# Kernel optimization log

Measured on AMD Instinct MI355X. Metric: run time of the kernel, lower is better.

The kernel has to match this reference:

```python
import jax, jax.numpy as jnp
import numpy as np
from jax import lax

NUM_SUPERNODES = 1024
KNN_K = 16
MIN_GRIPPER = 16
MIN_MASK = 8
GRIP_START = 0
GRIP_RADIUS = 0.1
NEG_INF = -jnp.inf


def _take(a, idx):
    return jnp.take_along_axis(a, idx, axis=1)


def _scatter_or(idx, keep, Bf, N):
    # OR `keep` into a fresh [Bf,N] bool mask at positions idx (mirrors torch scatter_)
    b = jnp.arange(Bf)[:, None]
    return jnp.zeros((Bf, N), dtype=bool).at[b, idx].max(keep)


def _cdist(a, b):
    # a [B,M,3], b [B,N,3] -> [B,M,N] euclidean
    d2 = (jnp.sum(a * a, -1)[:, :, None] + jnp.sum(b * b, -1)[:, None, :]
          - 2.0 * jnp.einsum('bmd,bnd->bmn', a, b))
    return jnp.sqrt(jnp.maximum(d2, 0.0))


def _sample_supernodes(xyz, valid, state, mask_id, extra_scores, global_scores):
    Bf, N, _ = xyz.shape
    M = NUM_SUPERNODES
    valid = valid.astype(bool)
    row_has_valid = valid.any(axis=1)
    first_valid = jnp.argmax(valid, axis=1).astype(jnp.int32)  # [Bf]

    # ---- gripper quota: nearest points to gripper xyz (within radius if any) ----
    k_grip = min(MIN_GRIPPER, M)
    gxyz = state[:, GRIP_START:GRIP_START + 3]
    gdist = jnp.linalg.norm(xyz - gxyz[:, None, :], axis=-1)  # [Bf,N]
    in_radius = gdist <= GRIP_RADIUS
    has_radius = (valid & in_radius).any(axis=1, keepdims=True)
    eligible = valid & (in_radius | ~has_radius)
    dist_rank = jnp.where(eligible, gdist, jnp.inf)
    neg_vals, grip_idx = lax.top_k(-dist_rank, k_grip)
    grip_vals = -neg_vals
    grip_keep = jnp.isfinite(grip_vals) & row_has_valid[:, None]
    head_idx = jnp.where(grip_keep, grip_idx, first_valid[:, None])
    head_bucket = jnp.where(grip_keep, 1, -1)
    selected = _scatter_or(grip_idx, grip_keep, Bf, N)

    remaining = M - k_grip
    # ---- mask-instance quota: one point per mask id (dedup via sort) ----
    mask_cand = valid & ~selected
    sentinel = jnp.iinfo(mask_id.dtype).max
    mask_key = jnp.where(mask_cand, mask_id, sentinel)
    sort_idx = jnp.argsort(mask_key, axis=1)
    sorted_valid = _take(mask_cand, sort_idx)
    sorted_mask = _take(mask_id, sort_idx)
    first_for_id = jnp.concatenate(
        [sorted_valid[:, :1],
         sorted_valid[:, 1:] & (sorted_mask[:, 1:] != sorted_mask[:, :-1])], axis=1)
    pos = jnp.arange(N, dtype=jnp.float32)[None, :]
    mask_scores = jnp.where(first_for_id, -pos, NEG_INF)
    mask_vals, mask_pos = lax.top_k(mask_scores, remaining)
    mask_idx = _take(sort_idx, mask_pos)
    mask_keep = jnp.isfinite(mask_vals) & row_has_valid[:, None]
    selected_after_mask = selected | _scatter_or(mask_idx, mask_keep, Bf, N)

    # ---- extra random mask supernodes to guarantee min_mask quota ----
    k_extra = min(MIN_MASK, remaining)
    es = jnp.where(valid & ~selected_after_mask, extra_scores, NEG_INF)
    extra_vals, extra_idx = lax.top_k(es, k_extra)
    extra_keep = jnp.isfinite(extra_vals) & row_has_valid[:, None]
    use_extra = ~mask_keep[:, :k_extra] & extra_keep
    mask_idx = mask_idx.at[:, :k_extra].set(
        jnp.where(use_extra, extra_idx, mask_idx[:, :k_extra]))
    mask_keep = mask_keep.at[:, :k_extra].set(mask_keep[:, :k_extra] | use_extra)

    # ---- global random fill ----
    selected_for_global = selected | _scatter_or(mask_idx, mask_keep, Bf, N)
    gs = jnp.where(valid & ~selected_for_global, global_scores, NEG_INF)
    gvals, gidx = lax.top_k(gs, remaining)
    gkeep = jnp.isfinite(gvals) & row_has_valid[:, None]
    fill_idx = jnp.where(mask_keep, mask_idx,
                         jnp.where(gkeep, gidx, first_valid[:, None]))
    fill_bucket = jnp.where(mask_keep, 2, jnp.where(gkeep, 0, -1))

    out_idx = jnp.concatenate([head_idx, fill_idx], axis=1)
    out_bucket = jnp.concatenate([head_bucket, fill_bucket], axis=1)
    out_valid = _take(valid, out_idx) & row_has_valid[:, None]
    out_bucket = jnp.where(out_valid, out_bucket, -1)
    return out_idx, out_valid, out_bucket


def setup_inputs() -> dict:
    key = jax.random.key(0)
    ks = jax.random.split(key, 6)
    Bf, N, C = 8, 16384, 64
    return {
        'x': jax.random.normal(ks[0], (Bf, N, C), dtype=jnp.float32),
        'xyz': jax.random.normal(ks[1], (Bf, N, 3), dtype=jnp.float32),
        'valid': jnp.ones((Bf, N), dtype=bool),
        'state': jax.random.normal(ks[2], (Bf, 8), dtype=jnp.float32),
        'mask_id': jax.random.randint(ks[3], (Bf, N), 0, 32, dtype=jnp.int32),
        'extra_scores': jax.random.uniform(ks[4], (Bf, N), dtype=jnp.float32),
        'global_scores': jax.random.uniform(ks[5], (Bf, N), dtype=jnp.float32),
    }


def reference(x, xyz, valid, state, mask_id, extra_scores, global_scores):
    Bf, N, C = x.shape
    out_idx, out_valid, out_bucket = _sample_supernodes(
        xyz, valid, state, mask_id, extra_scores, global_scores)
    # gather_points
    supernode_xyz = _take(xyz, out_idx[:, :, None].repeat(3, axis=2))  # [Bf,M,3]
    # build_knn_neighbors: masked cdist + topk smallest
    dist = _cdist(supernode_xyz.astype(jnp.float32), xyz.astype(jnp.float32))
    dist = jnp.where(valid.astype(bool)[:, None, :], dist, jnp.inf)
    neg_vals, neighbor_idx = lax.top_k(-dist, KNN_K)
    neighbor_mask = jnp.isfinite(-neg_vals)  # [Bf,M,K]
    # gather_neighbors
    b = jnp.arange(Bf)[:, None, None]
    neighbor_feats = x[b, neighbor_idx]  # [Bf,M,K,C]
    return (neighbor_feats, supernode_xyz, neighbor_mask,
            out_idx, out_valid, out_bucket)
```

## Files before the change

kernel.cpp:

```cpp
#include <hip/hip_runtime.h>
#include <math.h>

typedef unsigned long long u64;
typedef unsigned int u32;

#define BF 8
#define NPTS 16384
#define HALFPTS 8192
#define M_SN 1024
#define CCH 64
#define KNN 16
#define NTHR1 1024
#define KPER 16
#define TBL 4096
#define CCAP 2048
#define REM 1008

constexpr size_t O0 = 0;
constexpr size_t O1 = 8388608;
constexpr size_t O2 = 8413184;
constexpr size_t O3 = 8544256;
constexpr size_t O4 = 8552448;
constexpr size_t O5 = 8560640;

#define PW_OFF ((size_t)256)
#define PW_BYTES ((size_t)BF * NPTS * 16)
#define WN_BYTES ((size_t)2 * BF * M_SN * KNN * 8)

__device__ __forceinline__ bool is_valid_el(const void* vp, int mode, long long i) {
  if (mode == 1) return ((const unsigned char*)vp)[i] != 0;
  if (mode == 2) return ((const float*)vp)[i] != 0.0f;
  return ((const int*)vp)[i] != 0;
}

__device__ __forceinline__ u32 desc_enc(float f) {
  u32 u = __float_as_uint(f);
  u32 s = (u & 0x80000000u) ? ~u : (u | 0x80000000u);
  return ~s;
}
__device__ __forceinline__ bool enc_finite(u32 d) {
  u32 s = ~d;
  u32 u = (s & 0x80000000u) ? (s & 0x7FFFFFFFu) : ~s;
  return (u & 0x7F800000u) != 0x7F800000u;
}

__device__ __forceinline__ u64 wave_min_u64(u64 v) {
#pragma unroll
  for (int d = 32; d >= 1; d >>= 1) {
    u32 lo = __shfl_xor((u32)(v & 0xFFFFFFFFu), d, 64);
    u32 hi = __shfl_xor((u32)(v >> 32), d, 64);
    u64 o = ((u64)hi << 32) | lo;
    if (o < v) v = o;
  }
  return v;
}

__device__ __forceinline__ u64 block_min_u64(u64 v, u64* red16, int t) {
  v = wave_min_u64(v);
  if ((t & 63) == 0) red16[t >> 6] = v;
  __syncthreads();
  if (t < 64) {
    u64 x = red16[t & 15];
    x = wave_min_u64(x);
    if (t == 0) red16[0] = x;
  }
  __syncthreads();
  u64 r = red16[0];
  __syncthreads();
  return r;
}

__device__ __forceinline__ int block_excl_scan(int val, int* scanb, int t, int* tot) {
  int incl = val;
#pragma unroll
  for (int d = 1; d < 64; d <<= 1) {
    int v = __shfl_up(incl, d, 64);
    if ((t & 63) >= d) incl += v;
  }
  if ((t & 63) == 63) scanb[t >> 6] = incl;
  __syncthreads();
  if (t < 64) {
    int ws = (t < 16) ? scanb[t] : 0;
#pragma unroll
    for (int d = 1; d < 16; d <<= 1) {
      int v = __shfl_up(ws, d, 64);
      if ((t & 63) >= d) ws += v;
    }
    if (t < 16) scanb[16 + t] = ws;
  }
  __syncthreads();
  int wv = t >> 6;
  int base = (wv == 0) ? 0 : scanb[16 + wv - 1];
  *tot = scanb[16 + 15];
  int r = base + incl - val;
  __syncthreads();
  return r;
}

__device__ __forceinline__ u64 shfl64_grp(u64 v, int src) {
  u32 lo = (u32)__shfl((int)(u32)(v & 0xFFFFFFFFu), src, 32);
  u32 hi = (u32)__shfl((int)(u32)(v >> 32), src, 32);
  return ((u64)hi << 32) | lo;
}

template<bool ASC, bool SHIFTBIN>
__device__ __forceinline__ void topk_select(const u32* ek, const u32* bk, u32 cmask,
    int Twant, int* table, u64* cand, int* scanb, int* sh, int* outArr, int t) {
  for (int j = t; j < TBL; j += NTHR1) table[j] = 0;
  if (t == 6) sh[6] = 0x7FFFFFFF;
  if (t == 7) sh[7] = 1;
  __syncthreads();
#pragma unroll
  for (int k = 0; k < KPER; k++) {
    if ((cmask >> k) & 1u) {
      int bin = SHIFTBIN ? (int)(ek[k] >> 20) : (int)bk[k];
      atomicAdd(&table[bin], 1);
    }
  }
  __syncthreads();
  int c_[4]; int c4 = 0;
#pragma unroll
  for (int q = 0; q < 4; q++) { c_[q] = table[4 * t + q]; c4 += c_[q]; }
  int htot;
  int cum = block_excl_scan(c4, scanb, t, &htot);
  const int T = min(Twant, htot);
  int e_ = cum;
#pragma unroll
  for (int q = 0; q < 4; q++) {
    int nx = e_ + c_[q];
    if (T > 0 && e_ < T && nx >= T) atomicMin(&sh[6], 4 * t + q);
    table[4 * t + q] = e_;
    e_ = nx;
  }
  __syncthreads();
  if (T <= 0) return;
  const int B = sh[6];
#pragma unroll
  for (int k = 0; k < KPER; k++) {
    if ((cmask >> k) & 1u) {
      int bin = SHIFTBIN ? (int)(ek[k] >> 20) : (int)bk[k];
      if (bin <= B) {
        int pos = atomicAdd(&table[bin], 1);
        if (pos < CCAP)
          cand[pos] = ((u64)ek[k] << 32) | ((u64)(u32)bin << 14) | (u32)(k * NTHR1 + t);
      }
    }
  }
  __syncthreads();
  const int nc = table[B];
  if (nc <= CCAP) {
    for (int c = t; c < nc; c += NTHR1) {
      u64 key = cand[c];
      int bin = (int)((key >> 14) & 0xFFFu);
      int s = bin ? table[bin - 1] : 0;
      int e2 = table[bin];
      int r = s;
      for (int j = s; j < e2; j++) r += (cand[j] < key);
      if (r < T) {
        u32 enc = (u32)(key >> 32);
        int ix = (int)(key & 0x3FFFu);
        bool fin = ASC ? (enc < 0x7F800000u) : enc_finite(enc);
        outArr[r] = fin ? ix : (ix | (int)0x80000000);
      }
    }
  } else {
    if (t == 0) sh[7] = 0;
  }
  __syncthreads();
}

__global__ void detect_valid(const unsigned* __restrict__ w, int nwords, int* __restrict__ flag) {
  __shared__ int cls;
  int t = threadIdx.x;
  if (t == 0) cls = 0;
  __syncthreads();
  int local = 0;
  for (int i = t; i < nwords; i += blockDim.x) {
    unsigned v = w[i];
    if (v == 0x3F800000u) local = 2;
    else if (v != 0u && v != 1u) local = max(local, 1);
  }
  if (local) atomicMax(&cls, local);
  __syncthreads();
  if (t == 0) flag[0] = cls;
}

__global__ __launch_bounds__(1024)
void sample_kernel(const float* __restrict__ xyz, const void* __restrict__ validp,
                   const float* __restrict__ state, const int* __restrict__ mask_id,
                   const float* __restrict__ extra, const float* __restrict__ glob,
                   const int* __restrict__ flagp, float4* __restrict__ pw,
                   float* __restrict__ out) {
  __shared__ u64 red16[16];
  __shared__ int table[TBL];
  __shared__ int scanb[32];
  __shared__ int mpick[REM];
  __shared__ u64 cand[CCAP];
  __shared__ int gsorted[REM];
  __shared__ int head_i[16];
  __shared__ int head_bk[16];
  __shared__ int sh[8];

  const int b = blockIdx.x, t = threadIdx.x;
  const int vmode = flagp[0];
  const float* xyzb = xyz + (size_t)b * NPTS * 3;
  const int* midb = mask_id + (size_t)b * NPTS;
  const float* exb = extra + (size_t)b * NPTS;
  const float* glb = glob + (size_t)b * NPTS;

  if (t < 8) sh[t] = 0;
  if (t == 1) sh[1] = 0x7FFFFFFF;
  if (t < 16) gsorted[t] = -1;
  __syncthreads();

  u32 vbits = 0;
#pragma unroll
  for (int k = 0; k < KPER; k++) {
    int i = k * NTHR1 + t;
    if (is_valid_el(validp, vmode, (long long)b * NPTS + i)) vbits |= 1u << k;
  }
  if (vbits) {
    atomicOr(&sh[0], 1);
    atomicMin(&sh[1], (__ffs(vbits) - 1) * NTHR1 + t);
  }

  float gx = state[b * 8 + 0], gy = state[b * 8 + 1], gz = state[b * 8 + 2];
  float gd[KPER];
  u32 inr = 0;
#pragma unroll
  for (int k = 0; k < KPER; k++) {
    int i = k * NTHR1 + t;
    float px = xyzb[3 * i], py = xyzb[3 * i + 1], pz = xyzb[3 * i + 2];
    float dx = px - gx, dy = py - gy, dz = pz - gz;
    float d = sqrtf((dx * dx + dy * dy) + dz * dz);
    gd[k] = d;
    bool vb = (vbits >> k) & 1u;
    if (vb && d <= 0.1f) inr |= 1u << k;
    if (pw) {
      float sb = __fadd_rn(__fadd_rn(__fmul_rn(px, px), __fmul_rn(py, py)), __fmul_rn(pz, pz));
      pw[(size_t)b * NPTS + i] = make_float4(px, py, pz, vb ? sb : INFINITY);
    }
  }
  if (inr) atomicOr(&sh[2], 1);
  __syncthreads();

  const int rhv = sh[0];
  const int first_valid = rhv ? sh[1] : 0;
  const u32 elig = vbits & (sh[2] ? inr : 0xFFFFu);
  u32 sel = 0;

  {
    u32 ek[KPER];
#pragma unroll
    for (int k = 0; k < KPER; k++) ek[k] = __float_as_uint(gd[k]);
    topk_select<true, true>(ek, nullptr, elig, 16, table, cand, scanb, sh, gsorted, t);
    if (sh[7]) {
      if (t < 16) {
        int g = gsorted[t];
        head_i[t] = (g >= 0) ? g : first_valid;
        head_bk[t] = (g >= 0) ? 1 : -1;
      }
      __syncthreads();
      for (int j = 0; j < 16; j++) {
        if (head_bk[j] == 1) {
          int ix = head_i[j];
          if ((ix & (NTHR1 - 1)) == t) sel |= 1u << (ix >> 10);
        }
      }
    } else {
      for (int it = 0; it < 16; ++it) {
        u64 best = ~0ull;
#pragma unroll
        for (int k = 0; k < KPER; k++) {
          if (((elig >> k) & 1u) && !((sel >> k) & 1u)) {
            u64 key = ((u64)__float_as_uint(gd[k]) << 32) | (u32)(k * NTHR1 + t);
            if (key < best) best = key;
          }
        }
        u64 w = block_min_u64(best, red16, t);
        bool keep = (w >> 32) < 0x7F800000ull;
        int idx = (int)(w & 0xFFFFFFFFu);
        if (t == 0) { head_i[it] = keep ? idx : first_valid; head_bk[it] = keep ? 1 : -1; }
        if (keep && (idx & (NTHR1 - 1)) == t) sel |= 1u << (idx >> 10);
      }
      __syncthreads();
    }
  }

  for (int j = t; j < TBL; j += NTHR1) table[j] = 0x7FFFFFFF;
  __syncthreads();
#pragma unroll
  for (int k = 0; k < KPER; k++) {
    if (((vbits >> k) & 1u) && !((sel >> k) & 1u)) {
      int i = k * NTHR1 + t;
      int id = midb[i];
      if ((u32)id < TBL) atomicMin(&table[id], i);
    }
  }
  __syncthreads();
  int cnt = 0;
#pragma unroll
  for (int q = 0; q < 4; q++) cnt += (table[4 * t + q] != 0x7FFFFFFF);
  int mtot;
  int excl = block_excl_scan(cnt, scanb, t, &mtot);
  {
    int pos = excl;
#pragma unroll
    for (int q = 0; q < 4; q++) {
      int v = table[4 * t + q];
      if (v != 0x7FFFFFFF) { if (pos < REM) mpick[pos] = v; pos++; }
    }
  }
  __syncthreads();
  const int nm = min(mtot, REM);
  for (int j = 0; j < nm; j++) {
    int p = mpick[j];
    if ((p & (NTHR1 - 1)) == t) sel |= 1u << (p >> 10);
  }

  u32 extra_used = 0;
  if (nm < 8 && rhv) {
    u32 extrbits = 0;
    for (int j = 0; j < 8; j++) {
      u64 best = ~0ull;
#pragma unroll
      for (int k = 0; k < KPER; k++) {
        if (((vbits >> k) & 1u) && !((sel >> k) & 1u) && !((extrbits >> k) & 1u)) {
          int i = k * NTHR1 + t;
          u64 key = ((u64)desc_enc(exb[i]) << 32) | (u32)i;
          if (key < best) best = key;
        }
      }
      u64 w = block_min_u64(best, red16, t);
      if (w == ~0ull) break;
      int idx = (int)(w & 0xFFFFFFFFu);
      bool fin = enc_finite((u32)(w >> 32));
      if ((idx & (NTHR1 - 1)) == t) extrbits |= 1u << (idx >> 10);
      if (j >= nm && fin) {
        extra_used |= 1u << j;
        if (t == 0) mpick[j] = idx;
        if ((idx & (NTHR1 - 1)) == t) sel |= 1u << (idx >> 10);
      }
    }
    __syncthreads();
  }

  {
    u32 cbits = vbits & ~sel;
    u32 ek[KPER], bk[KPER];
#pragma unroll
    for (int k = 0; k < KPER; k++) {
      if ((cbits >> k) & 1u) {
        float f = glb[k * NTHR1 + t];
        ek[k] = desc_enc(f);
        float g = fminf(fmaxf(f, 0.0f), 0.99999994f);
        bk[k] = 4095u - (u32)(g * 4096.0f);
      } else { ek[k] = 0xFFFFFFFFu; bk[k] = 4095u; }
    }
    for (int j = t; j < REM; j += NTHR1) gsorted[j] = -1;
    topk_select<false, false>(ek, bk, cbits, REM, table, cand, scanb, sh, gsorted, t);
    if (!sh[7]) {
      u32 gext = 0;
      for (int j = 0; j < REM; j++) {
        u64 best = ~0ull;
#pragma unroll
        for (int k = 0; k < KPER; k++) {
          if (((cbits >> k) & 1u) && !((gext >> k) & 1u)) {
            u64 key = ((u64)ek[k] << 32) | (u32)(k * NTHR1 + t);
            if (key < best) best = key;
          }
        }
        u64 w = block_min_u64(best, red16, t);
        if (w == ~0ull) break;
        int idx = (int)(w & 0xFFFFFFFFu);
        if ((idx & (NTHR1 - 1)) == t) gext |= 1u << (idx >> 10);
        if (t == 0) gsorted[j] = enc_finite((u32)(w >> 32)) ? idx : (idx | (int)0x80000000);
      }
      __syncthreads();
    }
  }

  {
    int slot = t;
    int idx, bucket;
    if (slot < 16) {
      idx = head_i[slot];
      bucket = head_bk[slot];
    } else {
      int jj = slot - 16;
      bool mk = (jj < nm) || (jj < 8 && ((extra_used >> jj) & 1u));
      if (mk) { idx = mpick[jj]; bucket = 2; }
      else {
        int g = gsorted[jj];
        if (rhv && g >= 0) { idx = g; bucket = 0; }
        else { idx = first_valid; bucket = -1; }
      }
    }
    bool ov = rhv && is_valid_el(validp, vmode, (long long)b * NPTS + idx);
    int ob = ov ? bucket : -1;
    size_t o = (size_t)b * M_SN + slot;
    out[O3 + o] = (float)idx;
    out[O4 + o] = ov ? 1.0f : 0.0f;
    out[O5 + o] = (float)ob;
    out[O1 + 3 * o + 0] = xyzb[3 * idx + 0];
    out[O1 + 3 * o + 1] = xyzb[3 * idx + 1];
    out[O1 + 3 * o + 2] = xyzb[3 * idx + 2];
  }
}

#define NTHR2 256
#define CH 1024
#define SPB 8

__global__ __launch_bounds__(256, 8)
void knn_kernel(const float* __restrict__ x, const float* __restrict__ xyz,
                const void* __restrict__ validp, const int* __restrict__ flagp,
                const float4* __restrict__ pw, u64* __restrict__ wnws,
                float* __restrict__ out) {
  __shared__ __align__(16) float4 st[CH];
  __shared__ u64 wn[SPB * KNN];

  const int b = blockIdx.x >> 7;
  const int grp = blockIdx.x & 127;
  const int half = blockIdx.y;
  const int t = threadIdx.x;
  const int sl = t >> 5;
  const int sub = t & 31;
  const int lanebase = t & 32;
  const int m = grp * SPB + sl;
  const int vmode = flagp[0];
  const float* xyzb = xyz + (size_t)b * NPTS * 3;

  const int sidx = (int)out[O3 + (size_t)b * M_SN + m];
  float ax, ay, az;
  if (pw) { float4 q = pw[(size_t)b * NPTS + sidx]; ax = q.x; ay = q.y; az = q.z; }
  else { ax = xyzb[3 * sidx]; ay = xyzb[3 * sidx + 1]; az = xyzb[3 * sidx + 2]; }
  const float sa = __fadd_rn(__fadd_rn(__fmul_rn(ax, ax), __fmul_rn(ay, ay)), __fmul_rn(az, az));

  float ld2 = INFINITY;
  int lidx = 0;
  float kth = INFINITY;

  const int cbeg = wnws ? half * HALFPTS : 0;
  const int cend = wnws ? cbeg + HALFPTS : NPTS;

  for (int c0 = cbeg; c0 < cend; c0 += CH) {
    if (pw) {
      const float4* src = pw + (size_t)b * NPTS + c0;
#pragma unroll
      for (int q = 0; q < CH / NTHR2; q++) st[t + q * NTHR2] = src[t + q * NTHR2];
    } else {
      for (int p = t; p < CH; p += NTHR2) {
        float px = xyzb[3 * (c0 + p)], py = xyzb[3 * (c0 + p) + 1], pz = xyzb[3 * (c0 + p) + 2];
        bool v = is_valid_el(validp, vmode, (long long)b * NPTS + c0 + p);
        float sb = __fadd_rn(__fadd_rn(__fmul_rn(px, px), __fmul_rn(py, py)), __fmul_rn(pz, pz));
        st[p] = make_float4(px, py, pz, v ? sb : INFINITY);
      }
    }
    __syncthreads();
#pragma unroll 4
    for (int j = 0; j < CH / 32; j++) {
      float4 v = st[sub + 32 * j];
      float dot = __fadd_rn(__fadd_rn(__fmul_rn(ax, v.x), __fmul_rn(ay, v.y)), __fmul_rn(az, v.z));
      float d2 = fmaxf(__fsub_rn(__fadd_rn(sa, v.w), __fmul_rn(2.0f, dot)), 0.0f);
      u64 bal = __ballot(d2 < kth);
      u32 mq = (u32)(bal >> lanebase);
      while (mq) {
        int bb = __ffs(mq) - 1;
        mq &= mq - 1;
        float kd = __shfl(d2, lanebase + bb, 64);
        if (kd < kth) {
          int ki = c0 + 32 * j + bb;
          bool gt = ld2 > kd;
          float sd = __shfl_up(ld2, 1, 32);
          int si = __shfl_up(lidx, 1, 32);
          int pg = __shfl_up(gt ? 1 : 0, 1, 32);
          if (sub == 0) pg = 0;
          ld2 = gt ? (pg ? sd : kd) : ld2;
          lidx = gt ? (pg ? si : ki) : lidx;
          kth = __shfl(ld2, 15, 32);
        }
      }
    }
    __syncthreads();
  }

  if (wnws) {
    if (sub < KNN)
      wnws[((size_t)half * BF + b) * M_SN * KNN + (size_t)m * KNN + sub] =
          ((u64)__float_as_uint(ld2) << 32) | (u32)lidx;
    return;
  }

  if (sub < KNN) wn[sl * KNN + sub] = ((u64)__float_as_uint(ld2) << 32) | (u32)lidx;
  __syncthreads();
  {
    int s2 = t >> 5;
    int k2 = (t >> 1) & 15;
    int hf = t & 1;
    int mm = grp * SPB + s2;
    u64 key = wn[s2 * KNN + k2];
    int ni = (int)(key & (u64)(NPTS - 1));
    size_t o2 = ((size_t)b * M_SN + mm) * KNN + k2;
    if (hf == 0) out[O2 + o2] = ((u32)(key >> 32) < 0x7F800000u) ? 1.0f : 0.0f;
    const float4* src = (const float4*)(x + ((size_t)b * NPTS + ni) * CCH);
    float4* dst = (float4*)(out + O0 + o2 * CCH);
#pragma unroll
    for (int q = 0; q < 8; q++) dst[hf * 8 + q] = src[hf * 8 + q];
  }
}

__global__ __launch_bounds__(256)
void knn_merge_kernel(const float* __restrict__ x, const u64* __restrict__ wnws,
                      float* __restrict__ out) {
  __shared__ u64 wn[SPB * KNN];
  const int b = blockIdx.x >> 7;
  const int grp = blockIdx.x & 127;
  const int t = threadIdx.x;
  const int sl = t >> 5;
  const int sub = t & 31;
  const int m = grp * SPB + sl;

  const int h = sub >> 4, k = sub & 15;
  u64 my = wnws[((size_t)h * BF + b) * M_SN * KNN + (size_t)m * KNN + k];
  const int obase = (1 - h) << 4;
  int cnt2 = 0;
#pragma unroll
  for (int j = 0; j < 16; j++) {
    u64 o = shfl64_grp(my, obase + j);
    cnt2 += h ? (o <= my) : (o < my);
  }
  int rank = k + cnt2;
  if (rank < KNN) wn[sl * KNN + rank] = my;
  __syncthreads();

  {
    int s2 = t >> 5;
    int k2 = (t >> 1) & 15;
    int hf = t & 1;
    int mm = grp * SPB + s2;
    u64 key = wn[s2 * KNN + k2];
    int ni = (int)(key & (u64)(NPTS - 1));
    size_t o2 = ((size_t)b * M_SN + mm) * KNN + k2;
    if (hf == 0) out[O2 + o2] = ((u32)(key >> 32) < 0x7F800000u) ? 1.0f : 0.0f;
    const float4* src = (const float4*)(x + ((size_t)b * NPTS + ni) * CCH);
    float4* dst = (float4*)(out + O0 + o2 * CCH);
#pragma unroll
    for (int q = 0; q < 8; q++) dst[hf * 8 + q] = src[hf * 8 + q];
  }
}

extern "C" void kernel_launch(void* const* d_in, const int* in_sizes, int n_in,
                              void* d_out, int out_size, void* d_ws, size_t ws_size,
                              hipStream_t stream) {
  const float* x = (const float*)d_in[0];
  const float* xyz = (const float*)d_in[1];
  const void* valid = d_in[2];
  const float* state = (const float*)d_in[3];
  const int* mask_id = (const int*)d_in[4];
  const float* extra = (const float*)d_in[5];
  const float* glob = (const float*)d_in[6];
  float* out = (float*)d_out;
  int* flag = (int*)d_ws;

  float4* pw = nullptr;
  u64* wnws = nullptr;
  if (ws_size >= PW_OFF + PW_BYTES) pw = (float4*)((char*)d_ws + PW_OFF);
  if (pw && ws_size >= PW_OFF + PW_BYTES + WN_BYTES)
    wnws = (u64*)((char*)d_ws + PW_OFF + PW_BYTES);

  detect_valid<<<1, 1024, 0, stream>>>((const unsigned*)valid, in_sizes[2] / 4, flag);
  sample_kernel<<<BF, NTHR1, 0, stream>>>(xyz, valid, state, mask_id, extra, glob, flag, pw, out);
  dim3 kg(BF * 128, wnws ? 2 : 1);
  knn_kernel<<<kg, NTHR2, 0, stream>>>(x, xyz, valid, flag, pw, wnws, out);
  if (wnws) knn_merge_kernel<<<BF * 128, NTHR2, 0, stream>>>(x, wnws, out);
}
```

Measured before the change: 280.6 us.

## Rewrite KNN distance as FMA score and buffer candidates per chunk

The KNN scan now ranks points by the score 2a·p − |p|² computed with fused multiply-adds, in place of the full squared distance, so the ordering becomes a max-selection. The top-16 list is seeded from a sorting network over the first 32 points. Later candidates that beat the current threshold are appended to a per-group shared-memory buffer, which is merged after each chunk, with the old per-candidate insertion kept as a fallback when the buffer overflows. This is meant to cut the serialized shuffle-insertion work inside the inner loop, at the cost of extra shared memory, lower launch-bounds occupancy, a new key encoding (desc_enc/enc_finite), and possible rounding differences in tie ordering.

```diff
diff --git a/kernel.cpp b/kernel.cpp
--- a/kernel.cpp
+++ b/kernel.cpp
@@ -411,36 +411,42 @@
 #define NTHR2 256
 #define CH 1024
 #define SPB 8
-
-__global__ __launch_bounds__(256, 8)
+#define GCAP 64
+
+__global__ __launch_bounds__(256, 4)
 void knn_kernel(const float* __restrict__ x, const float* __restrict__ xyz,
                 const void* __restrict__ validp, const int* __restrict__ flagp,
                 const float4* __restrict__ pw, u64* __restrict__ wnws,
                 float* __restrict__ out) {
   __shared__ __align__(16) float4 st[CH];
+  __shared__ float bqf[(NTHR2 / 32) * GCAP];
+  __shared__ int bqi[(NTHR2 / 32) * GCAP];
   __shared__ u64 wn[SPB * KNN];
 
   const int b = blockIdx.x >> 7;
   const int grp = blockIdx.x & 127;
   const int half = blockIdx.y;
   const int t = threadIdx.x;
-  const int sl = t >> 5;
+  const int g = t >> 5;
   const int sub = t & 31;
   const int lanebase = t & 32;
-  const int m = grp * SPB + sl;
-  const int vmode = flagp[0];
+  const int m = grp * SPB + g;
   const float* xyzb = xyz + (size_t)b * NPTS * 3;
 
   const int sidx = (int)out[O3 + (size_t)b * M_SN + m];
   float ax, ay, az;
-  if (pw) { float4 q = pw[(size_t)b * NPTS + sidx]; ax = q.x; ay = q.y; az = q.z; }
+  if (pw) { float4 qv = pw[(size_t)b * NPTS + sidx]; ax = qv.x; ay = qv.y; az = qv.z; }
   else { ax = xyzb[3 * sidx]; ay = xyzb[3 * sidx + 1]; az = xyzb[3 * sidx + 2]; }
-  const float sa = __fadd_rn(__fadd_rn(__fmul_rn(ax, ax), __fmul_rn(ay, ay)), __fmul_rn(az, az));
-
-  float ld2 = INFINITY;
-  int lidx = 0;
-  float kth = INFINITY;
-
+  const float a2x = ax + ax, a2y = ay + ay, a2z = az + az;
+
+  float ld = -INFINITY;
+  int li = 0;
+  float kq = -INFINITY;
+  int bn = 0;
+  float* gbq = bqf + g * GCAP;
+  int* gbi = bqi + g * GCAP;
+
+  const int vmode = pw ? 0 : flagp[0];
   const int cbeg = wnws ? half * HALFPTS : 0;
   const int cend = wnws ? cbeg + HALFPTS : NPTS;
 
@@ -448,7 +454,7 @@
     if (pw) {
       const float4* src = pw + (size_t)b * NPTS + c0;
 #pragma unroll
-      for (int q = 0; q < CH / NTHR2; q++) st[t + q * NTHR2] = src[t + q * NTHR2];
+      for (int qq = 0; qq < CH / NTHR2; qq++) st[t + qq * NTHR2] = src[t + qq * NTHR2];
     } else {
       for (int p = t; p < CH; p += NTHR2) {
         float px = xyzb[3 * (c0 + p)], py = xyzb[3 * (c0 + p) + 1], pz = xyzb[3 * (c0 + p) + 2];
@@ -458,41 +464,96 @@
       }
     }
     __syncthreads();
+
+    int jstart = 0;
+    if (c0 == cbeg) {
+      float4 v = st[sub];
+      float qv = __builtin_fmaf(a2x, v.x, __builtin_fmaf(a2y, v.y, __builtin_fmaf(a2z, v.z, -v.w)));
+      int qi = c0 + sub;
+#pragma unroll
+      for (int p = 0; p < 32; p++) {
+        int par;
+        if ((p & 1) == 0) par = sub ^ 1;
+        else par = (sub == 0 || sub == 31) ? sub : (((sub - 1) ^ 1) + 1);
+        float oq = __shfl(qv, par, 32);
+        int oi = __shfl(qi, par, 32);
+        if (par != sub) {
+          bool lo = sub < par;
+          bool take = lo ? (oq > qv) : (oq < qv);
+          if (take) { qv = oq; qi = oi; }
+        }
+      }
+      ld = qv; li = qi;
+      kq = __shfl(ld, 15, 32);
+      jstart = 1;
+    }
+
 #pragma unroll 4
-    for (int j = 0; j < CH / 32; j++) {
+    for (int j = jstart; j < CH / 32; j++) {
       float4 v = st[sub + 32 * j];
-      float dot = __fadd_rn(__fadd_rn(__fmul_rn(ax, v.x), __fmul_rn(ay, v.y)), __fmul_rn(az, v.z));
-      float d2 = fmaxf(__fsub_rn(__fadd_rn(sa, v.w), __fmul_rn(2.0f, dot)), 0.0f);
-      u64 bal = __ballot(d2 < kth);
-      u32 mq = (u32)(bal >> lanebase);
-      while (mq) {
-        int bb = __ffs(mq) - 1;
-        mq &= mq - 1;
-        float kd = __shfl(d2, lanebase + bb, 64);
-        if (kd < kth) {
-          int ki = c0 + 32 * j + bb;
-          bool gt = ld2 > kd;
-          float sd = __shfl_up(ld2, 1, 32);
-          int si = __shfl_up(lidx, 1, 32);
+      float qv = __builtin_fmaf(a2x, v.x, __builtin_fmaf(a2y, v.y, __builtin_fmaf(a2z, v.z, -v.w)));
+      u64 bal = __ballot(qv > kq);
+      u32 mqg = (u32)(bal >> lanebase);
+      if (mqg) {
+        if (qv > kq) {
+          int pos = bn + __popc(mqg & ((1u << sub) - 1u));
+          if (pos < GCAP) { gbq[pos] = qv; gbi[pos] = c0 + 32 * j + sub; }
+        }
+        bn += __popc(mqg);
+      }
+    }
+
+    if (bn > GCAP) {
+      for (int j = jstart; j < CH / 32; j++) {
+        float4 v = st[sub + 32 * j];
+        float qv = __builtin_fmaf(a2x, v.x, __builtin_fmaf(a2y, v.y, __builtin_fmaf(a2z, v.z, -v.w)));
+        u64 bal = __ballot(qv > kq);
+        u32 mq = (u32)(bal >> lanebase);
+        while (mq) {
+          int bb = __ffs(mq) - 1;
+          mq &= mq - 1;
+          float kd = __shfl(qv, lanebase + bb, 64);
+          if (kd > kq) {
+            int ki = c0 + 32 * j + bb;
+            bool gt = ld < kd;
+            float sd = __shfl_up(ld, 1, 32);
+            int si = __shfl_up(li, 1, 32);
+            int pg = __shfl_up(gt ? 1 : 0, 1, 32);
+            if (sub == 0) pg = 0;
+            ld = gt ? (pg ? sd : kd) : ld;
+            li = gt ? (pg ? si : ki) : li;
+            kq = __shfl(ld, 15, 32);
+          }
+        }
+      }
+    } else {
+      for (int c = 0; c < bn; c++) {
+        float kd = gbq[c];
+        int ki = gbi[c];
+        if (kd > kq) {
+          bool gt = ld < kd;
+          float sd = __shfl_up(ld, 1, 32);
+          int si = __shfl_up(li, 1, 32);
           int pg = __shfl_up(gt ? 1 : 0, 1, 32);
           if (sub == 0) pg = 0;
-          ld2 = gt ? (pg ? sd : kd) : ld2;
-          lidx = gt ? (pg ? si : ki) : lidx;
-          kth = __shfl(ld2, 15, 32);
-        }
-      }
-    }
+          ld = gt ? (pg ? sd : kd) : ld;
+          li = gt ? (pg ? si : ki) : li;
+          kq = __shfl(ld, 15, 32);
+        }
+      }
+    }
+    bn = 0;
     __syncthreads();
   }
 
   if (wnws) {
     if (sub < KNN)
       wnws[((size_t)half * BF + b) * M_SN * KNN + (size_t)m * KNN + sub] =
-          ((u64)__float_as_uint(ld2) << 32) | (u32)lidx;
+          ((u64)desc_enc(ld) << 32) | (u32)li;
     return;
   }
 
-  if (sub < KNN) wn[sl * KNN + sub] = ((u64)__float_as_uint(ld2) << 32) | (u32)lidx;
+  if (sub < KNN) wn[g * KNN + sub] = ((u64)desc_enc(ld) << 32) | (u32)li;
   __syncthreads();
   {
     int s2 = t >> 5;
@@ -502,7 +563,7 @@
     u64 key = wn[s2 * KNN + k2];
     int ni = (int)(key & (u64)(NPTS - 1));
     size_t o2 = ((size_t)b * M_SN + mm) * KNN + k2;
-    if (hf == 0) out[O2 + o2] = ((u32)(key >> 32) < 0x7F800000u) ? 1.0f : 0.0f;
+    if (hf == 0) out[O2 + o2] = enc_finite((u32)(key >> 32)) ? 1.0f : 0.0f;
     const float4* src = (const float4*)(x + ((size_t)b * NPTS + ni) * CCH);
     float4* dst = (float4*)(out + O0 + o2 * CCH);
 #pragma unroll
@@ -542,7 +603,7 @@
     u64 key = wn[s2 * KNN + k2];
     int ni = (int)(key & (u64)(NPTS - 1));
     size_t o2 = ((size_t)b * M_SN + mm) * KNN + k2;
-    if (hf == 0) out[O2 + o2] = ((u32)(key >> 32) < 0x7F800000u) ? 1.0f : 0.0f;
+    if (hf == 0) out[O2 + o2] = enc_finite((u32)(key >> 32)) ? 1.0f : 0.0f;
     const float4* src = (const float4*)(x + ((size_t)b * NPTS + ni) * CCH);
     float4* dst = (float4*)(out + O0 + o2 * CCH);
 #pragma unroll
```

New measurement: 289.6 us. 1.03x slower.

## Register-block KNN over four supernodes per warp and split points into four segments

Applied to the files above, without the earlier changes.

The KNN kernel now processes four supernodes per 32-lane group and streams points straight from global memory with a one-step register prefetch, replacing the shared-memory staging and its barriers. It scores candidates with a fused 2a·b − |b|² FMA form, seeds each list with an odd-even transposition sort, and splits the point range into four segments, with a generalized rank-based merge kernel. The valid-type detection is folded into sample_kernel, which drops one launch. Reusing each loaded point across four supernodes cuts load traffic per distance, at the cost of more registers and a heavier merge step.

```diff
diff --git a/kernel.cpp b/kernel.cpp
--- a/kernel.cpp
+++ b/kernel.cpp
@@ -6,7 +6,6 @@
 
 #define BF 8
 #define NPTS 16384
-#define HALFPTS 8192
 #define M_SN 1024
 #define CCH 64
 #define KNN 16
@@ -25,7 +24,7 @@
 
 #define PW_OFF ((size_t)256)
 #define PW_BYTES ((size_t)BF * NPTS * 16)
-#define WN_BYTES ((size_t)2 * BF * M_SN * KNN * 8)
+#define SEG1_BYTES ((size_t)BF * M_SN * KNN * 8)
 
 __device__ __forceinline__ bool is_valid_el(const void* vp, int mode, long long i) {
   if (mode == 1) return ((const unsigned char*)vp)[i] != 0;
@@ -95,12 +94,6 @@
   int r = base + incl - val;
   __syncthreads();
   return r;
-}
-
-__device__ __forceinline__ u64 shfl64_grp(u64 v, int src) {
-  u32 lo = (u32)__shfl((int)(u32)(v & 0xFFFFFFFFu), src, 32);
-  u32 hi = (u32)__shfl((int)(u32)(v >> 32), src, 32);
-  return ((u64)hi << 32) | lo;
 }
 
 template<bool ASC, bool SHIFTBIN>
@@ -189,8 +182,7 @@
 void sample_kernel(const float* __restrict__ xyz, const void* __restrict__ validp,
                    const float* __restrict__ state, const int* __restrict__ mask_id,
                    const float* __restrict__ extra, const float* __restrict__ glob,
-                   const int* __restrict__ flagp, float4* __restrict__ pw,
-                   float* __restrict__ out) {
+                   int vwords, float4* __restrict__ pw, float* __restrict__ out) {
   __shared__ u64 red16[16];
   __shared__ int table[TBL];
   __shared__ int scanb[32];
@@ -202,7 +194,6 @@
   __shared__ int sh[8];
 
   const int b = blockIdx.x, t = threadIdx.x;
-  const int vmode = flagp[0];
   const float* xyzb = xyz + (size_t)b * NPTS * 3;
   const int* midb = mask_id + (size_t)b * NPTS;
   const float* exb = extra + (size_t)b * NPTS;
@@ -212,6 +203,19 @@
   if (t == 1) sh[1] = 0x7FFFFFFF;
   if (t < 16) gsorted[t] = -1;
   __syncthreads();
+
+  {
+    const unsigned* w = (const unsigned*)validp;
+    int local = 0;
+    for (int i = t; i < vwords; i += NTHR1) {
+      unsigned vv = w[i];
+      if (vv == 0x3F800000u) local = 2;
+      else if (vv != 0u && vv != 1u) local = max(local, 1);
+    }
+    if (local) atomicMax(&sh[3], local);
+  }
+  __syncthreads();
+  const int vmode = sh[3];
 
   u32 vbits = 0;
 #pragma unroll
@@ -409,144 +413,170 @@
 }
 
 #define NTHR2 256
-#define CH 1024
-#define SPB 8
-
-__global__ __launch_bounds__(256, 8)
+#define SPG 4
+#define SNBLK 32
+
+__device__ __forceinline__ float4 load_pt(const float4* pw, const float* xyzb,
+    const void* validp, int vmode, long long gbase, int i) {
+  if (pw) return pw[gbase + i];
+  float px = xyzb[3 * i], py = xyzb[3 * i + 1], pz = xyzb[3 * i + 2];
+  bool v = is_valid_el(validp, vmode, gbase + i);
+  float sb = __fadd_rn(__fadd_rn(__fmul_rn(px, px), __fmul_rn(py, py)), __fmul_rn(pz, pz));
+  return make_float4(px, py, pz, v ? sb : INFINITY);
+}
+
+__global__ __launch_bounds__(256)
 void knn_kernel(const float* __restrict__ x, const float* __restrict__ xyz,
                 const void* __restrict__ validp, const int* __restrict__ flagp,
-                const float4* __restrict__ pw, u64* __restrict__ wnws,
+                const float4* __restrict__ pw, u64* __restrict__ wnws, int nseg,
                 float* __restrict__ out) {
-  __shared__ __align__(16) float4 st[CH];
-  __shared__ u64 wn[SPB * KNN];
-
-  const int b = blockIdx.x >> 7;
-  const int grp = blockIdx.x & 127;
-  const int half = blockIdx.y;
+  __shared__ u64 wnl[SNBLK * KNN];
+
+  const int b = blockIdx.x >> 5;
+  const int snblk = blockIdx.x & 31;
+  const int seg = blockIdx.y;
   const int t = threadIdx.x;
-  const int sl = t >> 5;
+  const int g = t >> 5;
   const int sub = t & 31;
   const int lanebase = t & 32;
-  const int m = grp * SPB + sl;
-  const int vmode = flagp[0];
+  const int m0 = snblk * SNBLK + g * SPG;
   const float* xyzb = xyz + (size_t)b * NPTS * 3;
-
-  const int sidx = (int)out[O3 + (size_t)b * M_SN + m];
-  float ax, ay, az;
-  if (pw) { float4 q = pw[(size_t)b * NPTS + sidx]; ax = q.x; ay = q.y; az = q.z; }
-  else { ax = xyzb[3 * sidx]; ay = xyzb[3 * sidx + 1]; az = xyzb[3 * sidx + 2]; }
-  const float sa = __fadd_rn(__fadd_rn(__fmul_rn(ax, ax), __fmul_rn(ay, ay)), __fmul_rn(az, az));
-
-  float ld2 = INFINITY;
-  int lidx = 0;
-  float kth = INFINITY;
-
-  const int cbeg = wnws ? half * HALFPTS : 0;
-  const int cend = wnws ? cbeg + HALFPTS : NPTS;
-
-  for (int c0 = cbeg; c0 < cend; c0 += CH) {
-    if (pw) {
-      const float4* src = pw + (size_t)b * NPTS + c0;
-#pragma unroll
-      for (int q = 0; q < CH / NTHR2; q++) st[t + q * NTHR2] = src[t + q * NTHR2];
-    } else {
-      for (int p = t; p < CH; p += NTHR2) {
-        float px = xyzb[3 * (c0 + p)], py = xyzb[3 * (c0 + p) + 1], pz = xyzb[3 * (c0 + p) + 2];
-        bool v = is_valid_el(validp, vmode, (long long)b * NPTS + c0 + p);
-        float sb = __fadd_rn(__fadd_rn(__fmul_rn(px, px), __fmul_rn(py, py)), __fmul_rn(pz, pz));
-        st[p] = make_float4(px, py, pz, v ? sb : INFINITY);
-      }
-    }
-    __syncthreads();
-#pragma unroll 4
-    for (int j = 0; j < CH / 32; j++) {
-      float4 v = st[sub + 32 * j];
-      float dot = __fadd_rn(__fadd_rn(__fmul_rn(ax, v.x), __fmul_rn(ay, v.y)), __fmul_rn(az, v.z));
-      float d2 = fmaxf(__fsub_rn(__fadd_rn(sa, v.w), __fmul_rn(2.0f, dot)), 0.0f);
-      u64 bal = __ballot(d2 < kth);
+  const long long gbase = (long long)b * NPTS;
+  const int vmode = pw ? 0 : flagp[0];
+
+  float a2x[SPG], a2y[SPG], a2z[SPG];
+#pragma unroll
+  for (int s = 0; s < SPG; s++) {
+    int sidx = (int)out[O3 + (size_t)b * M_SN + m0 + s];
+    float ax, ay, az;
+    if (pw) { float4 c = pw[gbase + sidx]; ax = c.x; ay = c.y; az = c.z; }
+    else { ax = xyzb[3 * sidx]; ay = xyzb[3 * sidx + 1]; az = xyzb[3 * sidx + 2]; }
+    a2x[s] = ax + ax; a2y[s] = ay + ay; a2z[s] = az + az;
+  }
+
+  const int S = NPTS / nseg;
+  const int sbeg = seg * S;
+  const int NJ = S / 32;
+
+  float ld[SPG]; int li[SPG]; float kq[SPG];
+
+  {
+    float4 v = load_pt(pw, xyzb, validp, vmode, gbase, sbeg + sub);
+    float qv[SPG]; int qi[SPG];
+#pragma unroll
+    for (int s = 0; s < SPG; s++) {
+      qv[s] = __builtin_fmaf(a2x[s], v.x, __builtin_fmaf(a2y[s], v.y, __builtin_fmaf(a2z[s], v.z, -v.w)));
+      qi[s] = sbeg + sub;
+    }
+#pragma unroll
+    for (int p = 0; p < 32; p++) {
+      int par;
+      if ((p & 1) == 0) par = sub ^ 1;
+      else par = (sub == 0 || sub == 31) ? sub : (((sub - 1) ^ 1) + 1);
+      bool lo = sub < par;
+#pragma unroll
+      for (int s = 0; s < SPG; s++) {
+        float oq = __shfl(qv[s], par, 32);
+        int oi = __shfl(qi[s], par, 32);
+        if (par != sub) {
+          bool take = lo ? (oq > qv[s]) : (oq < qv[s]);
+          if (take) { qv[s] = oq; qi[s] = oi; }
+        }
+      }
+    }
+#pragma unroll
+    for (int s = 0; s < SPG; s++) { ld[s] = qv[s]; li[s] = qi[s]; kq[s] = __shfl(ld[s], 15, 32); }
+  }
+
+  float4 v = load_pt(pw, xyzb, validp, vmode, gbase, sbeg + 32 * (NJ > 1 ? 1 : 0) + sub);
+  for (int j = 1; j < NJ; j++) {
+    int jn = min(j + 1, NJ - 1);
+    float4 vn = load_pt(pw, xyzb, validp, vmode, gbase, sbeg + 32 * jn + sub);
+#pragma unroll
+    for (int s = 0; s < SPG; s++) {
+      float qv = __builtin_fmaf(a2x[s], v.x, __builtin_fmaf(a2y[s], v.y, __builtin_fmaf(a2z[s], v.z, -v.w)));
+      u64 bal = __ballot(qv > kq[s]);
       u32 mq = (u32)(bal >> lanebase);
       while (mq) {
         int bb = __ffs(mq) - 1;
         mq &= mq - 1;
-        float kd = __shfl(d2, lanebase + bb, 64);
-        if (kd < kth) {
-          int ki = c0 + 32 * j + bb;
-          bool gt = ld2 > kd;
-          float sd = __shfl_up(ld2, 1, 32);
-          int si = __shfl_up(lidx, 1, 32);
+        float kd = __shfl(qv, lanebase + bb, 64);
+        if (kd > kq[s]) {
+          int ki = sbeg + 32 * j + bb;
+          bool gt = ld[s] < kd;
+          float sd = __shfl_up(ld[s], 1, 32);
+          int si = __shfl_up(li[s], 1, 32);
           int pg = __shfl_up(gt ? 1 : 0, 1, 32);
           if (sub == 0) pg = 0;
-          ld2 = gt ? (pg ? sd : kd) : ld2;
-          lidx = gt ? (pg ? si : ki) : lidx;
-          kth = __shfl(ld2, 15, 32);
+          ld[s] = gt ? (pg ? sd : kd) : ld[s];
+          li[s] = gt ? (pg ? si : ki) : li[s];
+          kq[s] = __shfl(ld[s], 15, 32);
         }
       }
     }
-    __syncthreads();
+    v = vn;
   }
 
   if (wnws) {
-    if (sub < KNN)
-      wnws[((size_t)half * BF + b) * M_SN * KNN + (size_t)m * KNN + sub] =
-          ((u64)__float_as_uint(ld2) << 32) | (u32)lidx;
+#pragma unroll
+    for (int s = 0; s < SPG; s++)
+      if (sub < KNN)
+        wnws[(((size_t)seg * BF + b) * M_SN + (m0 + s)) * KNN + sub] =
+            ((u64)desc_enc(ld[s]) << 32) | (u32)li[s];
     return;
   }
 
-  if (sub < KNN) wn[sl * KNN + sub] = ((u64)__float_as_uint(ld2) << 32) | (u32)lidx;
+#pragma unroll
+  for (int s = 0; s < SPG; s++)
+    if (sub < KNN) wnl[(g * SPG + s) * KNN + sub] = ((u64)desc_enc(ld[s]) << 32) | (u32)li[s];
+  __syncthreads();
+  for (int r = t; r < SNBLK * KNN; r += NTHR2) {
+    u64 key = wnl[r];
+    int ni = (int)(key & (u64)(NPTS - 1));
+    int mm = snblk * SNBLK + (r >> 4);
+    size_t o2 = ((size_t)b * M_SN + mm) * KNN + (r & 15);
+    out[O2 + o2] = enc_finite((u32)(key >> 32)) ? 1.0f : 0.0f;
+    const float4* src = (const float4*)(x + (gbase + ni) * CCH);
+    float4* dst = (float4*)(out + O0 + o2 * CCH);
+#pragma unroll
+    for (int q = 0; q < 16; q++) dst[q] = src[q];
+  }
+}
+
+#define MSPB 4
+__global__ __launch_bounds__(256)
+void knn_merge_kernel(const float* __restrict__ x, const u64* __restrict__ wnws,
+                      int nseg, float* __restrict__ out) {
+  __shared__ u64 keys[MSPB][64];
+  __shared__ u64 wsel[MSPB][KNN];
+  const int b = blockIdx.x >> 8;
+  const int sn0 = (blockIdx.x & 255) * MSPB;
+  const int t = threadIdx.x;
+  const int s = t >> 6, e = t & 63;
+  const int E = nseg * KNN;
+  if (e < E) {
+    int seg = e >> 4, k = e & 15;
+    keys[s][e] = wnws[(((size_t)seg * BF + b) * M_SN + sn0 + s) * KNN + k];
+  }
+  __syncthreads();
+  if (e < E) {
+    u64 my = keys[s][e];
+    int rk = 0;
+    for (int j = 0; j < E; j++) rk += (keys[s][j] < my);
+    if (rk < KNN) wsel[s][rk] = my;
+  }
   __syncthreads();
   {
-    int s2 = t >> 5;
-    int k2 = (t >> 1) & 15;
-    int hf = t & 1;
-    int mm = grp * SPB + s2;
-    u64 key = wn[s2 * KNN + k2];
+    int row = t >> 2, q4 = t & 3;
+    u64 key = wsel[row >> 4][row & 15];
     int ni = (int)(key & (u64)(NPTS - 1));
-    size_t o2 = ((size_t)b * M_SN + mm) * KNN + k2;
-    if (hf == 0) out[O2 + o2] = ((u32)(key >> 32) < 0x7F800000u) ? 1.0f : 0.0f;
+    int mm = sn0 + (row >> 4);
+    size_t o2 = ((size_t)b * M_SN + mm) * KNN + (row & 15);
+    if (q4 == 0) out[O2 + o2] = enc_finite((u32)(key >> 32)) ? 1.0f : 0.0f;
     const float4* src = (const float4*)(x + ((size_t)b * NPTS + ni) * CCH);
     float4* dst = (float4*)(out + O0 + o2 * CCH);
 #pragma unroll
-    for (int q = 0; q < 8; q++) dst[hf * 8 + q] = src[hf * 8 + q];
-  }
-}
-
-__global__ __launch_bounds__(256)
-void knn_merge_kernel(const float* __restrict__ x, const u64* __restrict__ wnws,
-                      float* __restrict__ out) {
-  __shared__ u64 wn[SPB * KNN];
-  const int b = blockIdx.x >> 7;
-  const int grp = blockIdx.x & 127;
-  const int t = threadIdx.x;
-  const int sl = t >> 5;
-  const int sub = t & 31;
-  const int m = grp * SPB + sl;
-
-  const int h = sub >> 4, k = sub & 15;
-  u64 my = wnws[((size_t)h * BF + b) * M_SN * KNN + (size_t)m * KNN + k];
-  const int obase = (1 - h) << 4;
-  int cnt2 = 0;
-#pragma unroll
-  for (int j = 0; j < 16; j++) {
-    u64 o = shfl64_grp(my, obase + j);
-    cnt2 += h ? (o <= my) : (o < my);
-  }
-  int rank = k + cnt2;
-  if (rank < KNN) wn[sl * KNN + rank] = my;
-  __syncthreads();
-
-  {
-    int s2 = t >> 5;
-    int k2 = (t >> 1) & 15;
-    int hf = t & 1;
-    int mm = grp * SPB + s2;
-    u64 key = wn[s2 * KNN + k2];
-    int ni = (int)(key & (u64)(NPTS - 1));
-    size_t o2 = ((size_t)b * M_SN + mm) * KNN + k2;
-    if (hf == 0) out[O2 + o2] = ((u32)(key >> 32) < 0x7F800000u) ? 1.0f : 0.0f;
-    const float4* src = (const float4*)(x + ((size_t)b * NPTS + ni) * CCH);
-    float4* dst = (float4*)(out + O0 + o2 * CCH);
-#pragma unroll
-    for (int q = 0; q < 8; q++) dst[hf * 8 + q] = src[hf * 8 + q];
+    for (int q = 0; q < 4; q++) dst[q4 * 4 + q] = src[q4 * 4 + q];
   }
 }
 
@@ -562,16 +592,23 @@
   const float* glob = (const float*)d_in[6];
   float* out = (float*)d_out;
   int* flag = (int*)d_ws;
+  const int vwords = in_sizes[2] / 4;
 
   float4* pw = nullptr;
   u64* wnws = nullptr;
+  int nseg = 1;
   if (ws_size >= PW_OFF + PW_BYTES) pw = (float4*)((char*)d_ws + PW_OFF);
-  if (pw && ws_size >= PW_OFF + PW_BYTES + WN_BYTES)
-    wnws = (u64*)((char*)d_ws + PW_OFF + PW_BYTES);
-
-  detect_valid<<<1, 1024, 0, stream>>>((const unsigned*)valid, in_sizes[2] / 4, flag);
-  sample_kernel<<<BF, NTHR1, 0, stream>>>(xyz, valid, state, mask_id, extra, glob, flag, pw, out);
-  dim3 kg(BF * 128, wnws ? 2 : 1);
-  knn_kernel<<<kg, NTHR2, 0, stream>>>(x, xyz, valid, flag, pw, wnws, out);
-  if (wnws) knn_merge_kernel<<<BF * 128, NTHR2, 0, stream>>>(x, wnws, out);
-}
+  if (pw && ws_size >= PW_OFF + PW_BYTES + 4 * SEG1_BYTES) {
+    nseg = 4; wnws = (u64*)((char*)d_ws + PW_OFF + PW_BYTES);
+  } else if (pw && ws_size >= PW_OFF + PW_BYTES + 2 * SEG1_BYTES) {
+    nseg = 2; wnws = (u64*)((char*)d_ws + PW_OFF + PW_BYTES);
+  }
+
+  if (!pw)
+    detect_valid<<<1, 1024, 0, stream>>>((const unsigned*)valid, vwords, flag);
+  sample_kernel<<<BF, NTHR1, 0, stream>>>(xyz, valid, state, mask_id, extra, glob,
+                                          vwords, pw, out);
+  dim3 kg(BF * 32, nseg);
+  knn_kernel<<<kg, NTHR2, 0, stream>>>(x, xyz, valid, flag, pw, wnws, nseg, out);
+  if (nseg > 1) knn_merge_kernel<<<BF * 256, NTHR2, 0, stream>>>(x, wnws, nseg, out);
+}
```

Measured after the change: 310.7 us. 1.11x slower.
